# Kernel tuning notes

Measured on AMD Instinct MI355X. Metric: run time of the kernel, lower is better.

The kernel has to match this reference:

```python
import jax, jax.numpy as jnp
import numpy as np

EPS = 1e-08
KERNEL = 3


def setup_inputs() -> dict:
    key = jax.random.key(0)
    k1, k2, k3, k4 = jax.random.split(key, 4)
    N, IN_CH, OUT_CH, H, W, STYLE_DIM = 16, 256, 256, 64, 64, 512
    x = jax.random.normal(k1, (N, IN_CH, H, W), dtype=jnp.float32)
    style = jax.random.normal(k2, (N, STYLE_DIM), dtype=jnp.float32)
    # base weight: [1, out_ch, in_ch, k, k] (torch.randn init)
    weight = jax.random.normal(k3, (1, OUT_CH, IN_CH, KERNEL, KERNEL), dtype=jnp.float32)
    # modulation Linear(style_dim -> in_ch): weight ~ N(0,1), bias = 0
    mod_w = jax.random.normal(k4, (IN_CH, STYLE_DIM), dtype=jnp.float32)
    mod_b = jnp.zeros((IN_CH,), dtype=jnp.float32)
    return {"x": x, "style": style, "weight": weight, "mod_w": mod_w, "mod_b": mod_b}


def _per_sample_conv(xi, wi):
    # xi: [in_ch, H, W], wi: [out_ch, in_ch, k, k]
    pad = KERNEL // 2
    out = jax.lax.conv_general_dilated(
        xi[None], wi,
        window_strides=(1, 1),
        padding=[(pad, pad), (pad, pad)],
        dimension_numbers=("NCHW", "OIHW", "NCHW"),
    )
    return out[0]  # [out_ch, H, W]


def reference(x, style, weight, mod_w, mod_b):
    # modulation: Linear(style) -> [N, in_ch]
    s = style @ mod_w.T + mod_b  # [N, in_ch]
    # modulate base weight: [N, out_ch, in_ch, k, k]
    w = weight * (s[:, None, :, None, None] + 1.0)
    # demodulate
    demod = jax.lax.rsqrt(jnp.sum(w * w, axis=(2, 3, 4)) + EPS)  # [N, out_ch]
    w = w * demod[:, :, None, None, None]
    # grouped conv with groups=N == per-sample conv, vmapped over batch
    out = jax.vmap(_per_sample_conv)(x, w)  # [N, out_ch, H, W]
    return out
```

## Files before the change

kernel.cpp:

```cpp
#include <hip/hip_runtime.h>
#include <hip/hip_bf16.h>
#include <stdint.h>


#define NB  16
#define IC  256
#define OC  256
#define HW  64
#define HWP 66
#define SD  512
#define SPATIAL 4096
#define HWPIC 16896

typedef __hip_bfloat16 bf16;
typedef __bf16 bf16x8 __attribute__((ext_vector_type(8)));
typedef float  f32x4  __attribute__((ext_vector_type(4)));
typedef uint32_t u32a3 __attribute__((address_space(3)));
typedef const uint32_t u32a1 __attribute__((address_space(1)));

static __device__ __forceinline__ unsigned short f2bu(float f) {
    bf16 h = __float2bfloat16(f);
    union { bf16 b; unsigned short u; } c; c.b = h; return c.u;
}
static __device__ __forceinline__ void gll16(const void* g, void* l) {
    __builtin_amdgcn_global_load_lds((u32a1*)g, (u32a3*)l, 16, 0, 0);
}

__global__ __launch_bounds__(256)
void k_prep1(const float* __restrict__ weight, const float* __restrict__ style,
             const float* __restrict__ mod_w, const float* __restrict__ mod_b,
             float* __restrict__ wsq, bf16* __restrict__ wt2,
             uint4* __restrict__ xs4, float* __restrict__ scale) {
    int b = blockIdx.x, t = threadIdx.x;
    if (b < 256) {
        int tid = b * 256 + t;
        const float* wp = weight + (size_t)tid * 9;
        float v[9], s = 0.f;
        #pragma unroll
        for (int r = 0; r < 9; ++r) { v[r] = wp[r]; s += v[r] * v[r]; }
        wsq[tid] = s;
        #pragma unroll
        for (int r = 0; r < 9; ++r) wt2[(r << 16) + tid] = __float2bfloat16(v[r]);
    } else if (b < 784) {
        int idx = b - 256;
        int n = idx / 33, bx = idx - n * 33;
        int f = bx * 256 + t;
        int u = f >> 5, q = f & 31;
        if (u >= 260) return;
        int rb;
        if      (u <  66) rb = u;
        else if (u < 132) rb = 65 * 66 + (u - 66);
        else if (u < 196) rb = (u - 131) * 66;
        else              rb = (u - 195) * 66 + 65;
        xs4[(size_t)n * 139392 + rb * 32 + q] = make_uint4(0u, 0u, 0u, 0u);
    } else {
        int lane = t & 63;
        int w = (b - 784) * 4 + (t >> 6);
        int n = w >> 8, ic = w & 255;
        const float4* mw4 = (const float4*)mod_w + (size_t)ic * 128 + lane * 2;
        const float4* st4 = (const float4*)style + (size_t)n * 128 + lane * 2;
        float4 a0 = mw4[0], a1 = mw4[1], s0 = st4[0], s1 = st4[1];
        float acc = a0.x*s0.x + a0.y*s0.y + a0.z*s0.z + a0.w*s0.w
                  + a1.x*s1.x + a1.y*s1.y + a1.z*s1.z + a1.w*s1.w;
        #pragma unroll
        for (int off = 32; off > 0; off >>= 1) acc += __shfl_down(acc, off);
        if (lane == 0) scale[w] = acc + mod_b[ic] + 1.0f;
    }
}

__global__ __launch_bounds__(256)
void k_prep2(const float* __restrict__ x, const float* __restrict__ scale,
             const float* __restrict__ wsq, bf16* __restrict__ xs,
             float* __restrict__ demod) {
    __shared__ unsigned short tile[HW * 256];
    int b = blockIdx.x, t = threadIdx.x;
    if (b < 1024) {
        int y = b & 63, n = b >> 6;
        const float* sc = scale + n * IC;
        const float4* xp4 = (const float4*)(x + ((size_t)n * IC) * SPATIAL + (size_t)y * HW);
        #pragma unroll
        for (int i = 0; i < 16; ++i) {
            int fid = i * 256 + t;
            int ic = fid >> 4, f4 = fid & 15;
            float4 v = xp4[(size_t)ic * 1024 + f4];
            float s = sc[ic];
            int sp = f4 << 2;
            int sw = ic ^ ((f4 & 7) << 3);
            tile[(sp + 0) * 256 + sw] = f2bu(v.x * s);
            tile[(sp + 1) * 256 + sw] = f2bu(v.y * s);
            tile[(sp + 2) * 256 + sw] = f2bu(v.z * s);
            tile[(sp + 3) * 256 + sw] = f2bu(v.w * s);
        }
        __syncthreads();
        uint4* dst4 = (uint4*)(xs + (((size_t)n * HWP + (y + 1)) * HWP + 1) * IC);
        #pragma unroll
        for (int j = 0; j < 8; ++j) {
            int uid = j * 256 + t;
            int sp = uid >> 5, g = uid & 31;
            dst4[sp * 32 + g] =
                *(const uint4*)&tile[sp * 256 + ((g ^ ((sp >> 2) & 7)) << 3)];
        }
    } else {
        int n = b - 1024, oc = t;
        float* sc = (float*)tile;
        sc[t] = scale[n * IC + t];
        __syncthreads();
        const float4* wp4 = (const float4*)(wsq + (size_t)oc * IC);
        const float4* sc4 = (const float4*)sc;
        float acc = 0.f;
        #pragma unroll 8
        for (int i = 0; i < 64; ++i) {
            float4 q = wp4[i], s = sc4[i];
            acc += q.x*s.x*s.x + q.y*s.y*s.y + q.z*s.z*s.z + q.w*s.w*s.w;
        }
        demod[n * OC + oc] = rsqrtf(acc + 1e-8f);
    }
}

#define VM4 asm volatile("s_waitcnt vmcnt(4)" ::: "memory")
#define VM2 asm volatile("s_waitcnt vmcnt(2)" ::: "memory")
#define VM0 asm volatile("s_waitcnt vmcnt(0)" ::: "memory")
#define BAR __builtin_amdgcn_s_barrier()
#define SB0 __builtin_amdgcn_sched_barrier(0)

__global__ __launch_bounds__(512, 2)
void k_conv(const bf16* __restrict__ xs, const bf16* __restrict__ wt2,
            const float* __restrict__ demod, float* __restrict__ out) {
    extern __shared__ char smem[];
    int t = threadIdx.x, l = t & 63, w = t >> 6;
    int wm = w & 1, wn = w >> 1;
    int bid = blockIdx.x;
    int work = ((bid & 7) << 5) | (bid >> 3);
    int nimg = work >> 4;
    int ybase = (work & 15) << 2;
    int spb = (work & 15) << 8;

    int srow = (w << 3) + (l >> 3);
    int gseg = (l & 7) ^ (l >> 3);
    const bf16* gA = xs + (((size_t)nimg * HWP + ybase) * HWP + srow) * IC + (gseg << 3);
    const bf16* gB = wt2 + ((size_t)srow << 8) + (gseg << 3);
    int stW = w << 10;

    int aRow = ((wm << 6) + (l & 15)) << 7;
    int bRow = ((wn << 5) + (l & 15)) << 7;
    int sg0 = ((l >> 4) ^ (l & 7)) << 4;
    int sg1 = sg0 ^ 64;

    f32x4 acc[4][4][2];
    #pragma unroll
    for (int p = 0; p < 4; ++p)
        #pragma unroll
        for (int m = 0; m < 4; ++m)
            #pragma unroll
            for (int n = 0; n < 2; ++n) acc[p][m][n] = (f32x4){0.f, 0.f, 0.f, 0.f};

    bf16x8 afA[4][2], afB[4][2], bf0A[2][2], bf0B[2][2], bf1[2][2];

#define STG_A(ha, PARN, AOFF) do {                                          \
    const bf16* s_ = gA + (AOFF) + (ha) * 2 * HWPIC;                        \
    char* d_ = smem + (PARN) * 32768 + (ha) * 16384 + stW;                  \
    gll16(s_, d_); gll16(s_ + HWPIC, d_ + 8192); } while (0)
#define STG_B(hb, PARN, BOFF) do {                                          \
    const bf16* s_ = gB + (BOFF) + (hb) * (128 * IC);                       \
    char* d_ = smem + 65536 + (PARN) * 32768 + (hb) * 16384 + stW;          \
    gll16(s_, d_); gll16(s_ + 64 * IC, d_ + 8192); } while (0)
#define RD_A(DST, BASE) do { const char* A_ = (const char*)(BASE);          \
    _Pragma("unroll") for (int m_ = 0; m_ < 4; ++m_) {                      \
        DST[m_][0] = *(const bf16x8*)(A_ + m_ * 2048 + sg0);                \
        DST[m_][1] = *(const bf16x8*)(A_ + m_ * 2048 + sg1); } } while (0)
#define RD_B(DST, BASE) do { const char* B_ = (const char*)(BASE);          \
    _Pragma("unroll") for (int n_ = 0; n_ < 2; ++n_) {                      \
        DST[n_][0] = *(const bf16x8*)(B_ + n_ * 2048 + sg0);                \
        DST[n_][1] = *(const bf16x8*)(B_ + n_ * 2048 + sg1); } } while (0)
#define MM(P, AF, BF) do {                                                  \
    __builtin_amdgcn_s_setprio(1);                                          \
    _Pragma("unroll") for (int kk_ = 0; kk_ < 2; ++kk_)                     \
    _Pragma("unroll") for (int m_ = 0; m_ < 4; ++m_)                        \
    _Pragma("unroll") for (int n_ = 0; n_ < 2; ++n_)                        \
        acc[P][m_][n_] = __builtin_amdgcn_mfma_f32_16x16x32_bf16(           \
            AF[m_][kk_], BF[n_][kk_], acc[P][m_][n_], 0, 0, 0);             \
    __builtin_amdgcn_s_setprio(0); } while (0)

#define TILE(PAR, BF0C, BF0N, AOFF1, BOFF1) do {                            \
    const char* Ap_  = smem + (PAR) * 32768;                                \
    const char* Bp_  = smem + 65536 + (PAR) * 32768;                        \
    const char* Apn_ = smem + ((PAR) ^ 1) * 32768;                          \
    const char* Bpn_ = smem + 65536 + ((PAR) ^ 1) * 32768;                  \
     \
    STG_A(0, (PAR) ^ 1, AOFF1);                                             \
    VM4; BAR;                                                               \
    RD_B(bf1, Bp_ + 16384 + bRow);                                          \
    SB0;                                                                    \
    MM(0, afA, BF0C);                                                       \
                        \
    STG_B(0, (PAR) ^ 1, BOFF1);                                             \
    VM4; BAR;                                                               \
    RD_A(afB, Ap_ + 16384 + aRow);                                          \
    SB0;                                                                    \
    MM(1, afA, bf1);                                                        \
                                               \
    STG_B(1, (PAR) ^ 1, BOFF1);                                             \
    BAR;                                                                    \
    MM(2, afB, bf1);                                                        \
            \
    STG_A(1, (PAR) ^ 1, AOFF1);                                             \
    VM4; BAR;                                                               \
    RD_A(afA, Apn_ + aRow);                                                 \
    RD_B(BF0N, Bpn_ + bRow);                                                \
    SB0;                                                                    \
    MM(3, afB, BF0C);                                                       \
} while (0)

    STG_A(0, 0, 0);
    STG_B(0, 0, 0);
    STG_B(1, 0, 0);
    STG_A(1, 0, 0);
    VM4;
    BAR;
    RD_A(afA, smem + aRow);
    RD_B(bf0A, smem + 65536 + bRow);

    #pragma clang loop unroll(disable)
    for (int TT = 0; TT < 17; ++TT) {
        int Tn1 = 2 * TT + 1, Tn2 = 2 * TT + 2;
        int r1 = Tn1 >> 2, ic1 = (Tn1 & 3) << 6;
        int ky1 = r1 / 3, kx1 = r1 - ky1 * 3;
        int aoff1 = (ky1 * HWP + kx1) * IC + ic1, boff1 = (r1 << 16) + ic1;
        int r2 = Tn2 >> 2, ic2 = (Tn2 & 3) << 6;
        int ky2 = r2 / 3, kx2 = r2 - ky2 * 3;
        int aoff2 = (ky2 * HWP + kx2) * IC + ic2, boff2 = (r2 << 16) + ic2;
        TILE(0, bf0A, bf0B, aoff1, boff1);
        TILE(1, bf0B, bf0A, aoff2, boff2);
    }
    {
        int aoff35 = (2 * HWP + 2) * IC + 192, boff35 = (8 << 16) + 192;
        TILE(0, bf0A, bf0B, aoff35, boff35);
    }
    {
        const char* Ap_ = smem + 32768;
        const char* Bp_ = smem + 65536 + 32768;
        VM2; BAR;
        RD_B(bf1, Bp_ + 16384 + bRow);
        SB0;
        MM(0, afA, bf0B);
        VM0; BAR;
        RD_A(afB, Ap_ + 16384 + aRow);
        SB0;
        MM(1, afA, bf1);
        MM(2, afB, bf1);
        MM(3, afB, bf0B);
    }

    const float* dm = demod + nimg * OC;
    int ocol = l & 15, orow = (l >> 4) << 2;
    #pragma unroll
    for (int p = 0; p < 4; ++p) {
        int qa = p >> 1, qb = qa ^ (p & 1);
        #pragma unroll
        for (int n = 0; n < 2; ++n) {
            int oc = (qb << 7) + (wn << 5) + (n << 4) + ocol;
            float d = dm[oc];
            size_t ob = ((size_t)(nimg * OC + oc)) * SPATIAL
                      + spb + (qa << 7) + (wm << 6) + orow;
            #pragma unroll
            for (int m = 0; m < 4; ++m) {
                f32x4 a = acc[p][m][n];
                f32x4 o = { a[0] * d, a[1] * d, a[2] * d, a[3] * d };
                *reinterpret_cast<f32x4*>(out + ob + m * 16) = o;
            }
        }
    }
}

extern "C" void kernel_launch(void* const* d_in, const int* in_sizes, int n_in,
                              void* d_out, int out_size, void* d_ws, size_t ws_size,
                              hipStream_t stream) {
    const float* x      = (const float*)d_in[0];
    const float* style  = (const float*)d_in[1];
    const float* weight = (const float*)d_in[2];
    const float* mod_w  = (const float*)d_in[3];
    const float* mod_b  = (const float*)d_in[4];
    float* out = (float*)d_out;

    char* ws = (char*)d_ws;
    float* scale = (float*)(ws + 0);
    float* demod = (float*)(ws + 16384);
    float* wsq   = (float*)(ws + 32768);
    bf16*  wt2   = (bf16*)(ws + 294912);
    bf16*  xs    = (bf16*)(ws + 1474560);

    static int s_attr = 0;
    if (!s_attr) {
        hipFuncSetAttribute(reinterpret_cast<const void*>(k_conv),
                            hipFuncAttributeMaxDynamicSharedMemorySize, 131072);
        s_attr = 1;
    }

    k_prep1<<<1808, 256, 0, stream>>>(weight, style, mod_w, mod_b,
                                      wsq, wt2, (uint4*)xs, scale);
    k_prep2<<<1040, 256, 0, stream>>>(x, scale, wsq, xs, demod);
    k_conv<<<256, 512, 131072, stream>>>(xs, wt2, demod, out);
}
```

Baseline: 188.7 us.

## Merge prep kernels into one and compute demodulation inside conv kernel

The two preprocessing kernels become one launch: each of 256 blocks recomputes the style modulation scale for its image in shared memory and then converts four rows of x to padded bf16. Weight conversion and border zeroing run in other blocks of the same launch. The demod factors are now computed in the conv kernel's prologue while the first tile loads are in flight, which removes a kernel launch and a dependency boundary. In exchange, the modulation GEMV is repeated 16 times per image, and the conv prologue does extra global reads of wsq before the main loop. The x conversion is also spread over fewer blocks, each handling four rows serially.

```diff
diff --git a/kernel.cpp b/kernel.cpp
--- a/kernel.cpp
+++ b/kernel.cpp
@@ -27,13 +27,63 @@
 }
 
 __global__ __launch_bounds__(256)
-void k_prep1(const float* __restrict__ weight, const float* __restrict__ style,
-             const float* __restrict__ mod_w, const float* __restrict__ mod_b,
-             float* __restrict__ wsq, bf16* __restrict__ wt2,
-             uint4* __restrict__ xs4, float* __restrict__ scale) {
+void k_prep(const float* __restrict__ x, const float* __restrict__ style,
+            const float* __restrict__ weight, const float* __restrict__ mod_w,
+            const float* __restrict__ mod_b,
+            float* __restrict__ wsq, bf16* __restrict__ wt2,
+            bf16* __restrict__ xs, uint4* __restrict__ xs4,
+            float* __restrict__ scale) {
+    __shared__ float sty[SD];
+    __shared__ float sc[IC];
+    __shared__ unsigned short tile[HW * 256];
     int b = blockIdx.x, t = threadIdx.x;
     if (b < 256) {
-        int tid = b * 256 + t;
+        int n = b >> 4, yq = b & 15;
+        sty[t]       = style[n * SD + t];
+        sty[t + 256] = style[n * SD + 256 + t];
+        __syncthreads();
+        {
+            const float4* mw4 = (const float4*)mod_w + (size_t)t * 128;
+            const float4* st4 = (const float4*)sty;
+            float a = 0.f;
+            #pragma unroll 8
+            for (int j = 0; j < 128; ++j) {
+                float4 mv = mw4[j], sv = st4[j];
+                a += mv.x*sv.x + mv.y*sv.y + mv.z*sv.z + mv.w*sv.w;
+            }
+            sc[t] = a + mod_b[t] + 1.0f;
+            if (yq == 0) scale[n * IC + t] = sc[t];
+        }
+        __syncthreads();
+        for (int ry = 0; ry < 4; ++ry) {
+            int y = (yq << 2) + ry;
+            const float4* xp4 = (const float4*)(x + ((size_t)n * IC) * SPATIAL + (size_t)y * HW);
+            #pragma unroll
+            for (int i = 0; i < 16; ++i) {
+                int fid = i * 256 + t;
+                int ic = fid >> 4, f4 = fid & 15;
+                float4 v = xp4[(size_t)ic * 1024 + f4];
+                float s = sc[ic];
+                int sp = f4 << 2;
+                int sw = ic ^ ((f4 & 7) << 3);
+                tile[(sp + 0) * 256 + sw] = f2bu(v.x * s);
+                tile[(sp + 1) * 256 + sw] = f2bu(v.y * s);
+                tile[(sp + 2) * 256 + sw] = f2bu(v.z * s);
+                tile[(sp + 3) * 256 + sw] = f2bu(v.w * s);
+            }
+            __syncthreads();
+            uint4* dst4 = (uint4*)(xs + (((size_t)n * HWP + (y + 1)) * HWP + 1) * IC);
+            #pragma unroll
+            for (int j = 0; j < 8; ++j) {
+                int uid = j * 256 + t;
+                int sp = uid >> 5, g = uid & 31;
+                dst4[sp * 32 + g] =
+                    *(const uint4*)&tile[sp * 256 + ((g ^ ((sp >> 2) & 7)) << 3)];
+            }
+            __syncthreads();
+        }
+    } else if (b < 512) {
+        int tid = (b - 256) * 256 + t;
         const float* wp = weight + (size_t)tid * 9;
         float v[9], s = 0.f;
         #pragma unroll
@@ -41,8 +91,8 @@
         wsq[tid] = s;
         #pragma unroll
         for (int r = 0; r < 9; ++r) wt2[(r << 16) + tid] = __float2bfloat16(v[r]);
-    } else if (b < 784) {
-        int idx = b - 256;
+    } else {
+        int idx = b - 512;
         int n = idx / 33, bx = idx - n * 33;
         int f = bx * 256 + t;
         int u = f >> 5, q = f & 31;
@@ -53,67 +103,6 @@
         else if (u < 196) rb = (u - 131) * 66;
         else              rb = (u - 195) * 66 + 65;
         xs4[(size_t)n * 139392 + rb * 32 + q] = make_uint4(0u, 0u, 0u, 0u);
-    } else {
-        int lane = t & 63;
-        int w = (b - 784) * 4 + (t >> 6);
-        int n = w >> 8, ic = w & 255;
-        const float4* mw4 = (const float4*)mod_w + (size_t)ic * 128 + lane * 2;
-        const float4* st4 = (const float4*)style + (size_t)n * 128 + lane * 2;
-        float4 a0 = mw4[0], a1 = mw4[1], s0 = st4[0], s1 = st4[1];
-        float acc = a0.x*s0.x + a0.y*s0.y + a0.z*s0.z + a0.w*s0.w
-                  + a1.x*s1.x + a1.y*s1.y + a1.z*s1.z + a1.w*s1.w;
-        #pragma unroll
-        for (int off = 32; off > 0; off >>= 1) acc += __shfl_down(acc, off);
-        if (lane == 0) scale[w] = acc + mod_b[ic] + 1.0f;
-    }
-}
-
-__global__ __launch_bounds__(256)
-void k_prep2(const float* __restrict__ x, const float* __restrict__ scale,
-             const float* __restrict__ wsq, bf16* __restrict__ xs,
-             float* __restrict__ demod) {
-    __shared__ unsigned short tile[HW * 256];
-    int b = blockIdx.x, t = threadIdx.x;
-    if (b < 1024) {
-        int y = b & 63, n = b >> 6;
-        const float* sc = scale + n * IC;
-        const float4* xp4 = (const float4*)(x + ((size_t)n * IC) * SPATIAL + (size_t)y * HW);
-        #pragma unroll
-        for (int i = 0; i < 16; ++i) {
-            int fid = i * 256 + t;
-            int ic = fid >> 4, f4 = fid & 15;
-            float4 v = xp4[(size_t)ic * 1024 + f4];
-            float s = sc[ic];
-            int sp = f4 << 2;
-            int sw = ic ^ ((f4 & 7) << 3);
-            tile[(sp + 0) * 256 + sw] = f2bu(v.x * s);
-            tile[(sp + 1) * 256 + sw] = f2bu(v.y * s);
-            tile[(sp + 2) * 256 + sw] = f2bu(v.z * s);
-            tile[(sp + 3) * 256 + sw] = f2bu(v.w * s);
-        }
-        __syncthreads();
-        uint4* dst4 = (uint4*)(xs + (((size_t)n * HWP + (y + 1)) * HWP + 1) * IC);
-        #pragma unroll
-        for (int j = 0; j < 8; ++j) {
-            int uid = j * 256 + t;
-            int sp = uid >> 5, g = uid & 31;
-            dst4[sp * 32 + g] =
-                *(const uint4*)&tile[sp * 256 + ((g ^ ((sp >> 2) & 7)) << 3)];
-        }
-    } else {
-        int n = b - 1024, oc = t;
-        float* sc = (float*)tile;
-        sc[t] = scale[n * IC + t];
-        __syncthreads();
-        const float4* wp4 = (const float4*)(wsq + (size_t)oc * IC);
-        const float4* sc4 = (const float4*)sc;
-        float acc = 0.f;
-        #pragma unroll 8
-        for (int i = 0; i < 64; ++i) {
-            float4 q = wp4[i], s = sc4[i];
-            acc += q.x*s.x*s.x + q.y*s.y*s.y + q.z*s.z*s.z + q.w*s.w*s.w;
-        }
-        demod[n * OC + oc] = rsqrtf(acc + 1e-8f);
     }
 }
 
@@ -125,7 +114,8 @@
 
 __global__ __launch_bounds__(512, 2)
 void k_conv(const bf16* __restrict__ xs, const bf16* __restrict__ wt2,
-            const float* __restrict__ demod, float* __restrict__ out) {
+            const float* __restrict__ wsq, const float* __restrict__ scale,
+            float* __restrict__ out) {
     extern __shared__ char smem[];
     int t = threadIdx.x, l = t & 63, w = t >> 6;
     int wm = w & 1, wn = w >> 1;
@@ -145,6 +135,7 @@
     int bRow = ((wn << 5) + (l & 15)) << 7;
     int sg0 = ((l >> 4) ^ (l & 7)) << 4;
     int sg1 = sg0 ^ 64;
+    int ocol = l & 15;
 
     f32x4 acc[4][4][2];
     #pragma unroll
@@ -186,23 +177,19 @@
     const char* Bp_  = smem + 65536 + (PAR) * 32768;                        \
     const char* Apn_ = smem + ((PAR) ^ 1) * 32768;                          \
     const char* Bpn_ = smem + 65536 + ((PAR) ^ 1) * 32768;                  \
-     \
     STG_A(0, (PAR) ^ 1, AOFF1);                                             \
     VM4; BAR;                                                               \
     RD_B(bf1, Bp_ + 16384 + bRow);                                          \
     SB0;                                                                    \
     MM(0, afA, BF0C);                                                       \
-                        \
     STG_B(0, (PAR) ^ 1, BOFF1);                                             \
     VM4; BAR;                                                               \
     RD_A(afB, Ap_ + 16384 + aRow);                                          \
     SB0;                                                                    \
     MM(1, afA, bf1);                                                        \
-                                               \
     STG_B(1, (PAR) ^ 1, BOFF1);                                             \
     BAR;                                                                    \
     MM(2, afB, bf1);                                                        \
-            \
     STG_A(1, (PAR) ^ 1, AOFF1);                                             \
     VM4; BAR;                                                               \
     RD_A(afA, Apn_ + aRow);                                                 \
@@ -215,6 +202,31 @@
     STG_B(0, 0, 0);
     STG_B(1, 0, 0);
     STG_A(1, 0, 0);
+
+    float dmv[2][2];
+    {
+        const float4* scg  = (const float4*)(scale + (size_t)nimg * IC);
+        const float4* wq00 = (const float4*)(wsq + (size_t)((wn << 5) + ocol) * IC);
+        const float4* wq01 = (const float4*)(wsq + (size_t)((wn << 5) + 16 + ocol) * IC);
+        const float4* wq10 = (const float4*)(wsq + (size_t)(128 + (wn << 5) + ocol) * IC);
+        const float4* wq11 = (const float4*)(wsq + (size_t)(128 + (wn << 5) + 16 + ocol) * IC);
+        float a00 = 0.f, a01 = 0.f, a10 = 0.f, a11 = 0.f;
+        #pragma unroll 8
+        for (int i = 0; i < 64; ++i) {
+            float4 s = scg[i];
+            float sx = s.x*s.x, sy = s.y*s.y, sz = s.z*s.z, sw = s.w*s.w;
+            float4 q;
+            q = wq00[i]; a00 += q.x*sx + q.y*sy + q.z*sz + q.w*sw;
+            q = wq01[i]; a01 += q.x*sx + q.y*sy + q.z*sz + q.w*sw;
+            q = wq10[i]; a10 += q.x*sx + q.y*sy + q.z*sz + q.w*sw;
+            q = wq11[i]; a11 += q.x*sx + q.y*sy + q.z*sz + q.w*sw;
+        }
+        dmv[0][0] = rsqrtf(a00 + 1e-8f);
+        dmv[0][1] = rsqrtf(a01 + 1e-8f);
+        dmv[1][0] = rsqrtf(a10 + 1e-8f);
+        dmv[1][1] = rsqrtf(a11 + 1e-8f);
+    }
+
     VM4;
     BAR;
     RD_A(afA, smem + aRow);
@@ -251,15 +263,14 @@
         MM(3, afB, bf0B);
     }
 
-    const float* dm = demod + nimg * OC;
-    int ocol = l & 15, orow = (l >> 4) << 2;
+    int orow = (l >> 4) << 2;
     #pragma unroll
     for (int p = 0; p < 4; ++p) {
         int qa = p >> 1, qb = qa ^ (p & 1);
         #pragma unroll
         for (int n = 0; n < 2; ++n) {
             int oc = (qb << 7) + (wn << 5) + (n << 4) + ocol;
-            float d = dm[oc];
+            float d = dmv[qb][n];
             size_t ob = ((size_t)(nimg * OC + oc)) * SPATIAL
                       + spb + (qa << 7) + (wm << 6) + orow;
             #pragma unroll
@@ -284,7 +295,6 @@
 
     char* ws = (char*)d_ws;
     float* scale = (float*)(ws + 0);
-    float* demod = (float*)(ws + 16384);
     float* wsq   = (float*)(ws + 32768);
     bf16*  wt2   = (bf16*)(ws + 294912);
     bf16*  xs    = (bf16*)(ws + 1474560);
@@ -296,8 +306,7 @@
         s_attr = 1;
     }
 
-    k_prep1<<<1808, 256, 0, stream>>>(weight, style, mod_w, mod_b,
-                                      wsq, wt2, (uint4*)xs, scale);
-    k_prep2<<<1040, 256, 0, stream>>>(x, scale, wsq, xs, demod);
-    k_conv<<<256, 512, 131072, stream>>>(xs, wt2, demod, out);
-}
+    k_prep<<<1040, 256, 0, stream>>>(x, style, weight, mod_w, mod_b,
+                                     wsq, wt2, xs, (uint4*)xs, scale);
+    k_conv<<<256, 512, 131072, stream>>>(xs, wt2, wsq, scale, out);
+}
```

Result: slower. 293.7 us (+55.7%).

## Fuse prep kernels and bake modulation and demodulation into per-sample bf16 weights

Applied to the files above, without the earlier changes.

Adds a single prep kernel that computes style modulation, demodulation, per-sample modulated weights in bf16, and the padded channels-last input, replacing two prep launches with one. The conv kernel gets a template path that indexes per-sample weights and skips the demod scaling in the epilogue. This removes a kernel launch and the dependency between the prep stages. In exchange it writes 16x more weight data (about 19 MB) that the conv must stream from global memory rather than sharing one weight copy across images. The new path is chosen only when the workspace is large enough, with the old path kept as a fallback.

```diff
diff --git a/kernel.cpp b/kernel.cpp
--- a/kernel.cpp
+++ b/kernel.cpp
@@ -11,6 +11,7 @@
 #define SD  512
 #define SPATIAL 4096
 #define HWPIC 16896
+#define WT2N_STRIDE 589824
 
 typedef __hip_bfloat16 bf16;
 typedef __bf16 bf16x8 __attribute__((ext_vector_type(8)));
@@ -24,6 +25,118 @@
 }
 static __device__ __forceinline__ void gll16(const void* g, void* l) {
     __builtin_amdgcn_global_load_lds((u32a1*)g, (u32a3*)l, 16, 0, 0);
+}
+
+__global__ __launch_bounds__(256)
+void k_prepA(const float* __restrict__ x, const float* __restrict__ style,
+             const float* __restrict__ weight, const float* __restrict__ mod_w,
+             const float* __restrict__ mod_b,
+             bf16* __restrict__ wt2n, bf16* __restrict__ xs) {
+    __shared__ unsigned short tile[HW * 256];
+    int b = blockIdx.x, t = threadIdx.x;
+    if (b < 256) {
+        float* scL = (float*)tile;
+        float* red = scL + 256;
+        float* dm  = red + 256;
+        int n = b >> 4, ocb = (b & 15) << 4;
+        int l = t & 63, wv = t >> 6;
+        const float4* st4 = (const float4*)style + (size_t)n * 128 + (l << 1);
+        float4 s0 = st4[0], s1 = st4[1];
+        for (int g = 0; g < 64; g += 4) {
+            float av[4];
+            #pragma unroll
+            for (int k = 0; k < 4; ++k) {
+                int ic = (wv << 6) + g + k;
+                const float4* mw4 = (const float4*)mod_w + (size_t)ic * 128 + (l << 1);
+                float4 a0 = mw4[0], a1 = mw4[1];
+                av[k] = a0.x*s0.x + a0.y*s0.y + a0.z*s0.z + a0.w*s0.w
+                      + a1.x*s1.x + a1.y*s1.y + a1.z*s1.z + a1.w*s1.w;
+            }
+            #pragma unroll
+            for (int k = 0; k < 4; ++k) {
+                float a = av[k];
+                #pragma unroll
+                for (int off = 32; off > 0; off >>= 1) a += __shfl_down(a, off);
+                if (l == 0) {
+                    int ic = (wv << 6) + g + k;
+                    scL[ic] = a + mod_b[ic] + 1.0f;
+                }
+            }
+        }
+        __syncthreads();
+        int ocl = t >> 4, icg = t & 15;
+        int oc = ocb + ocl;
+        float accd = 0.f;
+        for (int i = 0; i < 16; ++i) {
+            int ic = (i << 4) + icg;
+            const float* wp = weight + ((size_t)oc * 256 + ic) * 9;
+            float s = scL[ic];
+            float sw = 0.f;
+            #pragma unroll
+            for (int r = 0; r < 9; ++r) { float v = wp[r]; sw += v * v; }
+            accd += sw * s * s;
+        }
+        red[t] = accd;
+        __syncthreads();
+        if (t < 16) {
+            float a = 0.f;
+            #pragma unroll
+            for (int j = 0; j < 16; ++j) a += red[(t << 4) + j];
+            dm[t] = rsqrtf(a + 1e-8f);
+        }
+        __syncthreads();
+        float dmo = dm[ocl];
+        const float* wrow = weight + (size_t)oc * 2304;
+        bf16* dst = wt2n + (size_t)n * WT2N_STRIDE + (size_t)oc * 256;
+        for (int r = 0; r < 9; ++r) {
+            unsigned short ob[16];
+            #pragma unroll
+            for (int i = 0; i < 16; ++i) {
+                int ic = (icg << 4) + i;
+                ob[i] = f2bu(wrow[ic * 9 + r] * scL[ic] * dmo);
+            }
+            uint4* d4 = (uint4*)(dst + (size_t)r * 65536 + (icg << 4));
+            d4[0] = *(uint4*)&ob[0];
+            d4[1] = *(uint4*)&ob[8];
+        }
+    } else if (b < 1280) {
+        int bb = b - 256, y = bb & 63, n = bb >> 6;
+        const float4* xp4 = (const float4*)(x + ((size_t)n * IC) * SPATIAL + (size_t)y * HW);
+        #pragma unroll
+        for (int i = 0; i < 16; ++i) {
+            int fid = i * 256 + t;
+            int ic = fid >> 4, f4 = fid & 15;
+            float4 v = xp4[(size_t)ic * 1024 + f4];
+            int sp = f4 << 2;
+            int sw = ic ^ ((f4 & 7) << 3);
+            tile[(sp + 0) * 256 + sw] = f2bu(v.x);
+            tile[(sp + 1) * 256 + sw] = f2bu(v.y);
+            tile[(sp + 2) * 256 + sw] = f2bu(v.z);
+            tile[(sp + 3) * 256 + sw] = f2bu(v.w);
+        }
+        __syncthreads();
+        uint4* dst4 = (uint4*)(xs + (((size_t)n * HWP + (y + 1)) * HWP + 1) * IC);
+        #pragma unroll
+        for (int j = 0; j < 8; ++j) {
+            int uid = j * 256 + t;
+            int sp = uid >> 5, g = uid & 31;
+            dst4[sp * 32 + g] =
+                *(const uint4*)&tile[sp * 256 + ((g ^ ((sp >> 2) & 7)) << 3)];
+        }
+    } else {
+        uint4* xs4 = (uint4*)xs;
+        int idx = b - 1280;
+        int n = idx / 33, bx = idx - n * 33;
+        int f = bx * 256 + t;
+        int u = f >> 5, q = f & 31;
+        if (u >= 260) return;
+        int rb;
+        if      (u <  66) rb = u;
+        else if (u < 132) rb = 65 * 66 + (u - 66);
+        else if (u < 196) rb = (u - 131) * 66;
+        else              rb = (u - 195) * 66 + 65;
+        xs4[(size_t)n * 139392 + rb * 32 + q] = make_uint4(0u, 0u, 0u, 0u);
+    }
 }
 
 __global__ __launch_bounds__(256)
@@ -123,6 +236,7 @@
 #define BAR __builtin_amdgcn_s_barrier()
 #define SB0 __builtin_amdgcn_sched_barrier(0)
 
+template<int PERN>
 __global__ __launch_bounds__(512, 2)
 void k_conv(const bf16* __restrict__ xs, const bf16* __restrict__ wt2,
             const float* __restrict__ demod, float* __restrict__ out) {
@@ -138,13 +252,15 @@
     int srow = (w << 3) + (l >> 3);
     int gseg = (l & 7) ^ (l >> 3);
     const bf16* gA = xs + (((size_t)nimg * HWP + ybase) * HWP + srow) * IC + (gseg << 3);
-    const bf16* gB = wt2 + ((size_t)srow << 8) + (gseg << 3);
+    const bf16* gB = wt2 + (PERN ? (size_t)nimg * WT2N_STRIDE : (size_t)0)
+                   + ((size_t)srow << 8) + (gseg << 3);
     int stW = w << 10;
 
     int aRow = ((wm << 6) + (l & 15)) << 7;
     int bRow = ((wn << 5) + (l & 15)) << 7;
     int sg0 = ((l >> 4) ^ (l & 7)) << 4;
     int sg1 = sg0 ^ 64;
+    int ocol = l & 15;
 
     f32x4 acc[4][4][2];
     #pragma unroll
@@ -186,23 +302,19 @@
     const char* Bp_  = smem + 65536 + (PAR) * 32768;                        \
     const char* Apn_ = smem + ((PAR) ^ 1) * 32768;                          \
     const char* Bpn_ = smem + 65536 + ((PAR) ^ 1) * 32768;                  \
-     \
     STG_A(0, (PAR) ^ 1, AOFF1);                                             \
     VM4; BAR;                                                               \
     RD_B(bf1, Bp_ + 16384 + bRow);                                          \
     SB0;                                                                    \
     MM(0, afA, BF0C);                                                       \
-                        \
     STG_B(0, (PAR) ^ 1, BOFF1);                                             \
     VM4; BAR;                                                               \
     RD_A(afB, Ap_ + 16384 + aRow);                                          \
     SB0;                                                                    \
     MM(1, afA, bf1);                                                        \
-                                               \
     STG_B(1, (PAR) ^ 1, BOFF1);                                             \
     BAR;                                                                    \
     MM(2, afB, bf1);                                                        \
-            \
     STG_A(1, (PAR) ^ 1, AOFF1);                                             \
     VM4; BAR;                                                               \
     RD_A(afA, Apn_ + aRow);                                                 \
@@ -251,15 +363,25 @@
         MM(3, afB, bf0B);
     }
 
-    const float* dm = demod + nimg * OC;
-    int ocol = l & 15, orow = (l >> 4) << 2;
+    float dmv[2][2];
+    if (PERN) {
+        dmv[0][0] = dmv[0][1] = dmv[1][0] = dmv[1][1] = 1.0f;
+    } else {
+        #pragma unroll
+        for (int qb = 0; qb < 2; ++qb)
+            #pragma unroll
+            for (int nn = 0; nn < 2; ++nn)
+                dmv[qb][nn] = demod[nimg * OC + (qb << 7) + (wn << 5) + (nn << 4) + ocol];
+    }
+
+    int orow = (l >> 4) << 2;
     #pragma unroll
     for (int p = 0; p < 4; ++p) {
         int qa = p >> 1, qb = qa ^ (p & 1);
         #pragma unroll
         for (int n = 0; n < 2; ++n) {
             int oc = (qb << 7) + (wn << 5) + (n << 4) + ocol;
-            float d = dm[oc];
+            float d = dmv[qb][n];
             size_t ob = ((size_t)(nimg * OC + oc)) * SPATIAL
                       + spb + (qa << 7) + (wm << 6) + orow;
             #pragma unroll
@@ -281,23 +403,35 @@
     const float* mod_w  = (const float*)d_in[3];
     const float* mod_b  = (const float*)d_in[4];
     float* out = (float*)d_out;
-
     char* ws = (char*)d_ws;
-    float* scale = (float*)(ws + 0);
-    float* demod = (float*)(ws + 16384);
-    float* wsq   = (float*)(ws + 32768);
-    bf16*  wt2   = (bf16*)(ws + 294912);
-    bf16*  xs    = (bf16*)(ws + 1474560);
 
     static int s_attr = 0;
     if (!s_attr) {
-        hipFuncSetAttribute(reinterpret_cast<const void*>(k_conv),
+        auto p0 = k_conv<0>; auto p1 = k_conv<1>;
+        hipFuncSetAttribute(reinterpret_cast<const void*>(p0),
+                            hipFuncAttributeMaxDynamicSharedMemorySize, 131072);
+        hipFuncSetAttribute(reinterpret_cast<const void*>(p1),
                             hipFuncAttributeMaxDynamicSharedMemorySize, 131072);
         s_attr = 1;
     }
 
-    k_prep1<<<1808, 256, 0, stream>>>(weight, style, mod_w, mod_b,
-                                      wsq, wt2, (uint4*)xs, scale);
-    k_prep2<<<1040, 256, 0, stream>>>(x, scale, wsq, xs, demod);
-    k_conv<<<256, 512, 131072, stream>>>(xs, wt2, demod, out);
-}
+    const size_t WT2N_BYTES = (size_t)NB * WT2N_STRIDE * 2;
+    const size_t XS_BYTES   = (size_t)NB * HWP * HWP * IC * 2;
+    if (ws_size >= WT2N_BYTES + XS_BYTES) {
+        bf16* wt2n = (bf16*)ws;
+        bf16* xs   = (bf16*)(ws + WT2N_BYTES);
+        k_prepA<<<1808, 256, 0, stream>>>(x, style, weight, mod_w, mod_b,
+                                          wt2n, xs);
+        k_conv<1><<<256, 512, 131072, stream>>>(xs, wt2n, nullptr, out);
+    } else {
+        float* scale = (float*)(ws + 0);
+        float* demod = (float*)(ws + 16384);
+        float* wsq   = (float*)(ws + 32768);
+        bf16*  wt2   = (bf16*)(ws + 294912);
+        bf16*  xs    = (bf16*)(ws + 1474560);
+        k_prep1<<<1808, 256, 0, stream>>>(weight, style, mod_w, mod_b,
+                                          wsq, wt2, (uint4*)xs, scale);
+        k_prep2<<<1040, 256, 0, stream>>>(x, scale, wsq, xs, demod);
+        k_conv<0><<<256, 512, 131072, stream>>>(xs, wt2, demod, out);
+    }
+}
```

Result: slower. 223.6 us (+18.5%).
